# Performance work log

Hardware: AMD Instinct MI355X
Metric: run time of the kernel (lower is better)

## Reference

```python
import jax
import jax.numpy as jnp
import numpy as np

H = 16  # n_heads
EPS = 1e-6


def setup_inputs() -> dict:
    key = jax.random.key(0)
    ks = jax.random.split(key, 7)
    B, L, D = 2, 1024, 1024
    w_scale = 1.0 / np.sqrt(D)
    return {
        "query": jax.random.normal(ks[0], (B, L, D), jnp.float32),
        "key": jax.random.normal(ks[1], (B, L, D), jnp.float32),
        "value": jax.random.normal(ks[2], (B, L, D), jnp.float32),
        "Wq": jax.random.normal(ks[3], (D, D), jnp.float32) * w_scale,
        "Wk": jax.random.normal(ks[4], (D, D), jnp.float32) * w_scale,
        "Wv": jax.random.normal(ks[5], (D, D), jnp.float32) * w_scale,
        "Wo": jax.random.normal(ks[6], (D, D), jnp.float32) * w_scale,
    }


def _phi(x):
    # elu feature map: elu(x) + 1 (always positive)
    return jax.nn.elu(x) + 1.0


def reference(query, key, value, Wq, Wk, Wv, Wo):
    B, L, D = query.shape
    d = D // H
    scale = d ** -0.5

    def proj(x, W):
        # [B,L,D] -> [B,H,L,d]
        return (x @ W.T).reshape(B, L, H, d).transpose(0, 2, 1, 3)

    q = proj(query, Wq) * scale
    k = proj(key, Wk) * scale
    v = proj(value, Wv)

    qp = _phi(q)  # [B,H,L,d]
    kp = _phi(k)

    # causal linear attention as a recurrence over time (same math as the
    # torch cumsum of k outer v, but without materializing [B,H,L,d,d])
    qs = jnp.moveaxis(qp, 2, 0)  # [L,B,H,d]
    ks = jnp.moveaxis(kp, 2, 0)
    vs = jnp.moveaxis(v, 2, 0)

    S0 = jnp.zeros((B, H, d, d), query.dtype)  # running sum of k outer v
    z0 = jnp.zeros((B, H, d), query.dtype)     # running sum of k'

    def step(carry, inp):
        S, z = carry
        qt, kt, vt = inp
        S = S + kt[..., :, None] * vt[..., None, :]  # [B,H,d,d]
        z = z + kt
        num = jnp.einsum('bhd,bhde->bhe', qt, S)
        den = jnp.einsum('bhd,bhd->bh', qt, z)[..., None]
        return (S, z), num / (den + EPS)

    _, out = jax.lax.scan(step, (S0, z0), (qs, ks, vs))  # out: [L,B,H,d]
    out = jnp.moveaxis(out, 0, 1).reshape(B, L, D)  # [B,L,D]
    # dropout is identity in eval mode
    return out @ Wo.T
```

## Files before the change

kernel.cpp:

```cpp
#include <hip/hip_runtime.h>
#include <hip/hip_bf16.h>
#include <math.h>

#define H_HEADS 16
#define DMODEL  1024
#define DHEAD   64
#define LSEQ    1024
#define CHUNK   64
#define NCHUNK  16
#define EPS_F   1e-6f

typedef __attribute__((ext_vector_type(8))) short bf16x8;
typedef __attribute__((ext_vector_type(4))) float f32x4;

__device__ inline unsigned short f2bf(float f) {
    unsigned int u = __float_as_uint(f);
    u += 0x7FFF + ((u >> 16) & 1);
    return (unsigned short)(u >> 16);
}
__device__ inline float bf2f(unsigned short h) {
    return __uint_as_float(((unsigned int)h) << 16);
}

__device__ inline int swz16(int row, int byteInRow) {
    return row * 128 + (byteInRow ^ ((row & 7) << 4));
}

#define GLOAD16(g, l) __builtin_amdgcn_global_load_lds( \
    (const __attribute__((address_space(1))) void*)(g), \
    (__attribute__((address_space(3))) void*)(l), 16, 0, 0)

__global__ __launch_bounds__(256)
void convert_kernel(const float* __restrict__ q, const float* __restrict__ k,
                    const float* __restrict__ v,
                    const float* __restrict__ Wq, const float* __restrict__ Wk,
                    const float* __restrict__ Wv, const float* __restrict__ Wo,
                    unsigned short* __restrict__ Xb, unsigned short* __restrict__ Wb)
{
    const int y = blockIdx.y;
    const float* src;
    unsigned short* dst;
    int n;
    if (y < 3) {
        src = (y == 0) ? q : (y == 1) ? k : v;
        dst = Xb + (size_t)y * (2 * LSEQ * DMODEL);
        n = 2 * LSEQ * DMODEL;
    } else {
        int w = y - 3;
        src = (w == 0) ? Wq : (w == 1) ? Wk : (w == 2) ? Wv : Wo;
        dst = Wb + (size_t)w * (DMODEL * DMODEL);
        n = DMODEL * DMODEL;
    }
    int idx = (blockIdx.x * 256 + threadIdx.x) * 4;
    if (idx < n) {
        float4 f = *(const float4*)(src + idx);
        ushort4 h = make_ushort4(f2bf(f.x), f2bf(f.y), f2bf(f.z), f2bf(f.w));
        *(ushort4*)(dst + idx) = h;
    }
}

template<bool PROJ>
__global__ __launch_bounds__(256)
void mfma_gemm64_kernel(const unsigned short* __restrict__ Xb,
                        const unsigned short* __restrict__ Wb,
                        unsigned short* __restrict__ qp,
                        unsigned short* __restrict__ kp,
                        unsigned short* __restrict__ vp,
                        float* __restrict__ outf)
{
    const int z = PROJ ? blockIdx.z : 0;
    const unsigned short* X = PROJ ? (Xb + (size_t)z * (2 * LSEQ * DMODEL)) : Xb;
    const unsigned short* W = PROJ ? (Wb + (size_t)z * (DMODEL * DMODEL)) : Wb;

    __shared__ unsigned short As[2 * 64 * 32];
    __shared__ unsigned short Bs[2 * 128 * 32];

    const int tid  = threadIdx.x;
    const int m0   = blockIdx.y * 64;
    const int n0   = blockIdx.x * 128;
    const int lane = tid & 63;
    const int wid  = tid >> 6;
    const int wm   = (wid >> 1) * 32;
    const int wn   = (wid & 1) * 64;
    const int r16  = lane & 15;
    const int qh   = lane >> 4;

    const int rA  = wid * 16 + (lane >> 2);
    const int rB0 = wid * 32 + (lane >> 2);
    const int sw  = ((lane & 3) ^ ((lane >> 3) & 3)) * 16;
    const char* srcA  = (const char*)(X + (size_t)(m0 + rA)  * DMODEL) + sw;
    const char* srcB0 = (const char*)(W + (size_t)(n0 + rB0) * DMODEL) + sw;
    const char* srcB1 = (const char*)(W + (size_t)(n0 + rB0 + 16) * DMODEL) + sw;
    char* dstA  = (char*)As + wid * 1024;
    char* dstB0 = (char*)Bs + wid * 2048;
    char* dstB1 = (char*)Bs + wid * 2048 + 1024;

    const int sl = (qh ^ ((r16 >> 1) & 3)) * 8;

    f32x4 acc[2][4];
#pragma unroll
    for (int i = 0; i < 2; ++i)
#pragma unroll
        for (int j = 0; j < 4; ++j) acc[i][j] = (f32x4)0.0f;

    for (int kt = 0; kt < DMODEL; kt += 64) {
#pragma unroll
        for (int hh = 0; hh < 2; ++hh) {
            size_t go = (size_t)(kt + hh * 32) * 2;
            GLOAD16(srcA  + go, dstA  + hh * 4096);
            GLOAD16(srcB0 + go, dstB0 + hh * 8192);
            GLOAD16(srcB1 + go, dstB1 + hh * 8192);
        }
        __syncthreads();

        bf16x8 af[2][2], bg[2][4];
#pragma unroll
        for (int hh = 0; hh < 2; ++hh) {
#pragma unroll
            for (int fm = 0; fm < 2; ++fm)
                af[hh][fm] = *(const bf16x8*)&As[hh * 2048 + (wm + fm * 16 + r16) * 32 + sl];
#pragma unroll
            for (int fn = 0; fn < 4; ++fn)
                bg[hh][fn] = *(const bf16x8*)&Bs[hh * 4096 + (wn + fn * 16 + r16) * 32 + sl];
        }
#pragma unroll
        for (int hh = 0; hh < 2; ++hh)
#pragma unroll
            for (int fm = 0; fm < 2; ++fm)
#pragma unroll
                for (int fn = 0; fn < 4; ++fn)
                    acc[fm][fn] = __builtin_amdgcn_mfma_f32_16x16x32_bf16(
                        af[hh][fm], bg[hh][fn], acc[fm][fn], 0, 0, 0);
        __syncthreads();
    }

    if (PROJ) {
        unsigned short* O = (z == 0) ? qp : (z == 1) ? kp : vp;
        const float sc = (z < 2) ? 0.125f : 1.f;
#pragma unroll
        for (int fm = 0; fm < 2; ++fm) {
#pragma unroll
            for (int r = 0; r < 4; ++r) {
                int m = m0 + wm + fm * 16 + qh * 4 + r;
                int b = m >> 10, l = m & 1023;
#pragma unroll
                for (int fn = 0; fn < 4; ++fn) {
                    int n = n0 + wn + fn * 16 + r16;
                    int h = n >> 6, e = n & 63;
                    float y = acc[fm][fn][r] * sc;
                    if (z < 2) y = (y > 0.f) ? y + 1.f : __expf(y);
                    O[(((size_t)(b * H_HEADS + h)) * LSEQ + l) * DHEAD + e] = f2bf(y);
                }
            }
        }
    } else {
#pragma unroll
        for (int fm = 0; fm < 2; ++fm) {
#pragma unroll
            for (int r = 0; r < 4; ++r) {
                int m = m0 + wm + fm * 16 + qh * 4 + r;
#pragma unroll
                for (int fn = 0; fn < 4; ++fn) {
                    int n = n0 + wn + fn * 16 + r16;
                    outf[(size_t)m * DMODEL + n] = acc[fm][fn][r];
                }
            }
        }
    }
}

__global__ __launch_bounds__(256)
void chunk_kv_kernel(const unsigned short* __restrict__ kp,
                     const unsigned short* __restrict__ vp,
                     float* __restrict__ St, float* __restrict__ z)
{
    const int c = blockIdx.x, bh = blockIdx.y;
    const int tid = threadIdx.x;
    const int lane = tid & 63;
    const int w = tid >> 6;
    const int r16 = lane & 15, qh = lane >> 4;

    __shared__ unsigned short kT[64 * 64];
    __shared__ unsigned short vt[64 * 64];

    const size_t base = ((size_t)bh * LSEQ + (size_t)c * CHUNK) * DHEAD;

#pragma unroll
    for (int i = 0; i < 2; ++i) {
        int id  = tid + i * 256;
        int row = id >> 3;
        int cg  = (id & 7) * 8;
        bf16x8 kv = *(const bf16x8*)(kp + base + row * 64 + cg);
        bf16x8 vv = *(const bf16x8*)(vp + base + row * 64 + cg);
#pragma unroll
        for (int j = 0; j < 8; ++j) {
            *(unsigned short*)((char*)kT + swz16(cg + j, row * 2)) = (unsigned short)kv[j];
            *(unsigned short*)((char*)vt + swz16(cg + j, row * 2)) = (unsigned short)vv[j];
        }
    }
    __syncthreads();

    bf16x8 av[2], bK[2][4];
#pragma unroll
    for (int kk = 0; kk < 2; ++kk) {
        av[kk] = *(const bf16x8*)((char*)vt + swz16(w * 16 + r16, kk * 64 + qh * 16));
#pragma unroll
        for (int fn = 0; fn < 4; ++fn)
            bK[kk][fn] = *(const bf16x8*)((char*)kT + swz16(fn * 16 + r16, kk * 64 + qh * 16));
    }

    f32x4 acc[4];
#pragma unroll
    for (int fn = 0; fn < 4; ++fn) acc[fn] = (f32x4)0.0f;
#pragma unroll
    for (int kk = 0; kk < 2; ++kk)
#pragma unroll
        for (int fn = 0; fn < 4; ++fn)
            acc[fn] = __builtin_amdgcn_mfma_f32_16x16x32_bf16(av[kk], bK[kk][fn], acc[fn], 0, 0, 0);

    const size_t sbase = ((size_t)bh * NCHUNK + c) * (DHEAD * DHEAD);
#pragma unroll
    for (int r = 0; r < 4; ++r) {
        int e = w * 16 + qh * 4 + r;
#pragma unroll
        for (int fn = 0; fn < 4; ++fn)
            St[sbase + (size_t)e * 64 + fn * 16 + r16] = acc[fn][r];
    }

    if (w == 0) {
        bf16x8 ones;
#pragma unroll
        for (int j = 0; j < 8; ++j) ones[j] = (short)0x3F80;
        f32x4 accz[4];
#pragma unroll
        for (int fn = 0; fn < 4; ++fn) accz[fn] = (f32x4)0.0f;
#pragma unroll
        for (int kk = 0; kk < 2; ++kk)
#pragma unroll
            for (int fn = 0; fn < 4; ++fn)
                accz[fn] = __builtin_amdgcn_mfma_f32_16x16x32_bf16(ones, bK[kk][fn], accz[fn], 0, 0, 0);
        if (qh == 0) {
            const size_t zb = ((size_t)bh * NCHUNK + c) * 64;
#pragma unroll
            for (int fn = 0; fn < 4; ++fn)
                z[zb + fn * 16 + r16] = accz[fn][0];
        }
    }
}

__global__ __launch_bounds__(256)
void prefix_kernel(const float* __restrict__ St, unsigned short* __restrict__ stb,
                   float* __restrict__ z)
{
    const int bh   = blockIdx.x >> 4;
    const int eblk = blockIdx.x & 15;
    const int idx  = eblk * 256 + threadIdx.x;
    const int e = idx >> 6, i = idx & 63;

    const size_t ibase = (size_t)bh * NCHUNK * 4096 + idx;
    float v[NCHUNK];
#pragma unroll
    for (int c = 0; c < NCHUNK; ++c)
        v[c] = St[ibase + (size_t)c * 4096];

    const size_t obase = (size_t)bh * NCHUNK * 4096 + e * 64 + (i ^ ((e & 7) << 3));
    float run = 0.f;
#pragma unroll
    for (int c = 0; c < NCHUNK; ++c) {
        stb[obase + (size_t)c * 4096] = f2bf(run);
        run += v[c];
    }

    if (eblk == 0 && threadIdx.x < DHEAD) {
        const size_t zb = (size_t)bh * NCHUNK * DHEAD + threadIdx.x;
        float zv[NCHUNK];
#pragma unroll
        for (int c = 0; c < NCHUNK; ++c)
            zv[c] = z[zb + (size_t)c * DHEAD];
        float zr = 0.f;
#pragma unroll
        for (int c = 0; c < NCHUNK; ++c) {
            z[zb + (size_t)c * DHEAD] = zr;
            zr += zv[c];
        }
    }
}

__global__ __launch_bounds__(256)
void attn_mfma_kernel(const unsigned short* __restrict__ qp,
                      const unsigned short* __restrict__ kp,
                      const unsigned short* __restrict__ vp,
                      const unsigned short* __restrict__ stb,
                      const float* __restrict__ zpre,
                      unsigned short* __restrict__ att)
{
    const int c = blockIdx.x, bh = blockIdx.y;
    const int b = bh >> 4, h = bh & 15;
    const int tid = threadIdx.x;
    const int lane = tid & 63;
    const int w = tid >> 6;
    const int r16 = lane & 15, qh = lane >> 4;

    __shared__ unsigned short qs[64 * 64];
    __shared__ unsigned short ks[64 * 64];
    __shared__ unsigned short vt[64 * 64];
    __shared__ unsigned short stl[64 * 64];
    __shared__ unsigned short ps[64 * 64];
    __shared__ float denl[64];

    const size_t base = ((size_t)bh * LSEQ + (size_t)c * CHUNK) * DHEAD;
    const unsigned short* stg = stb + ((size_t)bh * NCHUNK + c) * 4096;
    const float* zp = zpre + ((size_t)bh * NCHUNK + c) * 64;

    {
        const char* src = (const char*)stg + w * 2048 + lane * 16;
        GLOAD16(src,        (char*)stl + w * 2048);
        GLOAD16(src + 1024, (char*)stl + w * 2048 + 1024);
    }
#pragma unroll
    for (int i = 0; i < 2; ++i) {
        int id  = tid + i * 256;
        int row = id >> 3;
        int cg  = (id & 7) * 8;
        bf16x8 qv = *(const bf16x8*)(qp + base + row * 64 + cg);
        bf16x8 kv = *(const bf16x8*)(kp + base + row * 64 + cg);
        *(bf16x8*)((char*)qs + swz16(row, cg * 2)) = qv;
        *(bf16x8*)((char*)ks + swz16(row, cg * 2)) = kv;
        bf16x8 vv = *(const bf16x8*)(vp + base + row * 64 + cg);
#pragma unroll
        for (int j = 0; j < 8; ++j)
            *(unsigned short*)((char*)vt + swz16(cg + j, row * 2)) = (unsigned short)vv[j];
    }
    {
        int t = tid >> 2, kq = tid & 3;
        const unsigned short* qrow = qp + base + t * 64 + kq * 16;
        bf16x8 a0 = *(const bf16x8*)(qrow);
        bf16x8 a1 = *(const bf16x8*)(qrow + 8);
        float s = 0.f;
#pragma unroll
        for (int j = 0; j < 8; ++j) {
            s = fmaf(bf2f((unsigned short)a0[j]), zp[kq * 16 + j], s);
            s = fmaf(bf2f((unsigned short)a1[j]), zp[kq * 16 + 8 + j], s);
        }
        s += __shfl_xor(s, 1);
        s += __shfl_xor(s, 2);
        if (kq == 0) denl[t] = s;
    }
    __syncthreads();

    bf16x8 aq[2];
#pragma unroll
    for (int kk = 0; kk < 2; ++kk)
        aq[kk] = *(const bf16x8*)((char*)qs + swz16(w * 16 + r16, kk * 64 + qh * 16));

    f32x4 accp[4];
#pragma unroll
    for (int fn = 0; fn < 4; ++fn) accp[fn] = (f32x4)0.0f;
#pragma unroll
    for (int kk = 0; kk < 2; ++kk)
#pragma unroll
        for (int fn = 0; fn < 4; ++fn) {
            bf16x8 bk = *(const bf16x8*)((char*)ks + swz16(fn * 16 + r16, kk * 64 + qh * 16));
            accp[fn] = __builtin_amdgcn_mfma_f32_16x16x32_bf16(aq[kk], bk, accp[fn], 0, 0, 0);
        }

    float rs[4];
#pragma unroll
    for (int r = 0; r < 4; ++r) {
        int t_loc = w * 16 + qh * 4 + r;
        float rsum = 0.f;
#pragma unroll
        for (int fn = 0; fn < 4; ++fn) {
            int s_loc = fn * 16 + r16;
            float p = (s_loc <= t_loc) ? accp[fn][r] : 0.f;
            rsum += p;
            *(unsigned short*)((char*)ps + swz16(t_loc, s_loc * 2)) = f2bf(p);
        }
        rsum += __shfl_xor(rsum, 1);
        rsum += __shfl_xor(rsum, 2);
        rsum += __shfl_xor(rsum, 4);
        rsum += __shfl_xor(rsum, 8);
        rs[r] = rsum;
    }

    f32x4 acc[4];
#pragma unroll
    for (int fn = 0; fn < 4; ++fn) acc[fn] = (f32x4)0.0f;
#pragma unroll
    for (int kk = 0; kk < 2; ++kk)
#pragma unroll
        for (int fn = 0; fn < 4; ++fn) {
            bf16x8 bs = *(const bf16x8*)((char*)stl + swz16(fn * 16 + r16, kk * 64 + qh * 16));
            acc[fn] = __builtin_amdgcn_mfma_f32_16x16x32_bf16(aq[kk], bs, acc[fn], 0, 0, 0);
        }
    bf16x8 ap[2];
#pragma unroll
    for (int kk = 0; kk < 2; ++kk)
        ap[kk] = *(const bf16x8*)((char*)ps + swz16(w * 16 + r16, kk * 64 + qh * 16));
#pragma unroll
    for (int kk = 0; kk < 2; ++kk)
#pragma unroll
        for (int fn = 0; fn < 4; ++fn) {
            bf16x8 bv = *(const bf16x8*)((char*)vt + swz16(fn * 16 + r16, kk * 64 + qh * 16));
            acc[fn] = __builtin_amdgcn_mfma_f32_16x16x32_bf16(ap[kk], bv, acc[fn], 0, 0, 0);
        }

#pragma unroll
    for (int r = 0; r < 4; ++r) {
        int t_loc = w * 16 + qh * 4 + r;
        int l = c * CHUNK + t_loc;
        float inv = 1.f / (denl[t_loc] + rs[r] + EPS_F);
#pragma unroll
        for (int fn = 0; fn < 4; ++fn) {
            int e = fn * 16 + r16;
            att[((size_t)b * LSEQ + l) * DMODEL + h * DHEAD + e] = f2bf(acc[fn][r] * inv);
        }
    }
}

extern "C" void kernel_launch(void* const* d_in, const int* in_sizes, int n_in,
                              void* d_out, int out_size, void* d_ws, size_t ws_size,
                              hipStream_t stream)
{
    const float* query = (const float*)d_in[0];
    const float* key_  = (const float*)d_in[1];
    const float* value = (const float*)d_in[2];
    const float* Wq = (const float*)d_in[3];
    const float* Wk = (const float*)d_in[4];
    const float* Wv = (const float*)d_in[5];
    const float* Wo = (const float*)d_in[6];
    float* out = (float*)d_out;

    const int M  = 2 * LSEQ;
    const int BH = 2 * H_HEADS;

    char* wsb = (char*)d_ws;
    unsigned short* Wb   = (unsigned short*)(wsb);
    unsigned short* qp   = (unsigned short*)(wsb + 8388608);
    unsigned short* kp   = (unsigned short*)(wsb + 12582912);
    unsigned short* vp   = (unsigned short*)(wsb + 16777216);
    unsigned short* attb = (unsigned short*)(wsb + 20971520);
    unsigned short* Xb   = (unsigned short*)(wsb + 25165824);
    float*          St   = (float*)(wsb + 25165824);
    float*          z    = (float*)(wsb + 33554432);
    unsigned short* stb  = (unsigned short*)(wsb + 33685504);

    dim3 blk(256);
    convert_kernel<<<dim3(2048, 7), blk, 0, stream>>>(
        query, key_, value, Wq, Wk, Wv, Wo, Xb, Wb);
    mfma_gemm64_kernel<true><<<dim3(DMODEL / 128, M / 64, 3), blk, 0, stream>>>(
        Xb, Wb, qp, kp, vp, nullptr);
    chunk_kv_kernel<<<dim3(NCHUNK, BH), blk, 0, stream>>>(kp, vp, St, z);
    prefix_kernel<<<dim3(BH * 16), blk, 0, stream>>>(St, stb, z);
    attn_mfma_kernel<<<dim3(NCHUNK, BH), blk, 0, stream>>>(qp, kp, vp, stb, z, attb);
    mfma_gemm64_kernel<false><<<dim3(DMODEL / 128, M / 64, 1), blk, 0, stream>>>(
        attb, Wb + 3 * (size_t)DMODEL * DMODEL, nullptr, nullptr, nullptr, out);
}
```

Measured before the change: 74.78 us.

## Double-buffer LDS tiles in MFMA GEMM to overlap global loads with compute

Splits the shared-memory A/B tiles into two buffers and issues direct global-to-LDS loads for the next K tile before running the MFMA work on the current one, with a single barrier per iteration. This is meant to hide global load latency behind matrix math in the projection and output GEMMs. It doubles LDS use per block, which may lower occupancy, and relies on hand-placed waitcnt and scheduling barriers being correct.

```diff
diff --git a/kernel.cpp b/kernel.cpp
--- a/kernel.cpp
+++ b/kernel.cpp
@@ -72,8 +72,8 @@
     const unsigned short* X = PROJ ? (Xb + (size_t)z * (2 * LSEQ * DMODEL)) : Xb;
     const unsigned short* W = PROJ ? (Wb + (size_t)z * (DMODEL * DMODEL)) : Wb;
 
-    __shared__ unsigned short As[2 * 64 * 32];
-    __shared__ unsigned short Bs[2 * 128 * 32];
+    __shared__ char AsB[2][8192];
+    __shared__ char BsB[2][16384];
 
     const int tid  = threadIdx.x;
     const int m0   = blockIdx.y * 64;
@@ -91,9 +91,6 @@
     const char* srcA  = (const char*)(X + (size_t)(m0 + rA)  * DMODEL) + sw;
     const char* srcB0 = (const char*)(W + (size_t)(n0 + rB0) * DMODEL) + sw;
     const char* srcB1 = (const char*)(W + (size_t)(n0 + rB0 + 16) * DMODEL) + sw;
-    char* dstA  = (char*)As + wid * 1024;
-    char* dstB0 = (char*)Bs + wid * 2048;
-    char* dstB1 = (char*)Bs + wid * 2048 + 1024;
 
     const int sl = (qh ^ ((r16 >> 1) & 3)) * 8;
 
@@ -103,25 +100,27 @@
 #pragma unroll
         for (int j = 0; j < 4; ++j) acc[i][j] = (f32x4)0.0f;
 
-    for (int kt = 0; kt < DMODEL; kt += 64) {
+    auto STAGE = [&](int buf, int kt) {
 #pragma unroll
         for (int hh = 0; hh < 2; ++hh) {
             size_t go = (size_t)(kt + hh * 32) * 2;
-            GLOAD16(srcA  + go, dstA  + hh * 4096);
-            GLOAD16(srcB0 + go, dstB0 + hh * 8192);
-            GLOAD16(srcB1 + go, dstB1 + hh * 8192);
-        }
-        __syncthreads();
-
+            GLOAD16(srcA  + go, AsB[buf] + wid * 1024 + hh * 4096);
+            GLOAD16(srcB0 + go, BsB[buf] + wid * 2048 + hh * 8192);
+            GLOAD16(srcB1 + go, BsB[buf] + wid * 2048 + 1024 + hh * 8192);
+        }
+    };
+    auto COMPUTE = [&](int buf) {
         bf16x8 af[2][2], bg[2][4];
 #pragma unroll
         for (int hh = 0; hh < 2; ++hh) {
 #pragma unroll
             for (int fm = 0; fm < 2; ++fm)
-                af[hh][fm] = *(const bf16x8*)&As[hh * 2048 + (wm + fm * 16 + r16) * 32 + sl];
+                af[hh][fm] = *(const bf16x8*)(AsB[buf] + hh * 4096 +
+                                 ((wm + fm * 16 + r16) * 32 + sl) * 2);
 #pragma unroll
             for (int fn = 0; fn < 4; ++fn)
-                bg[hh][fn] = *(const bf16x8*)&Bs[hh * 4096 + (wn + fn * 16 + r16) * 32 + sl];
+                bg[hh][fn] = *(const bf16x8*)(BsB[buf] + hh * 8192 +
+                                 ((wn + fn * 16 + r16) * 32 + sl) * 2);
         }
 #pragma unroll
         for (int hh = 0; hh < 2; ++hh)
@@ -131,8 +130,24 @@
                 for (int fn = 0; fn < 4; ++fn)
                     acc[fm][fn] = __builtin_amdgcn_mfma_f32_16x16x32_bf16(
                         af[hh][fm], bg[hh][fn], acc[fm][fn], 0, 0, 0);
-        __syncthreads();
-    }
+    };
+
+    STAGE(0, 0);
+    asm volatile("s_waitcnt vmcnt(0)" ::: "memory");
+    __builtin_amdgcn_s_barrier();
+
+    int cur = 0;
+#pragma unroll 1
+    for (int t = 0; t < (DMODEL / 64) - 1; ++t) {
+        STAGE(cur ^ 1, (t + 1) * 64);
+        __builtin_amdgcn_sched_barrier(0);
+        COMPUTE(cur);
+        asm volatile("s_waitcnt vmcnt(0) lgkmcnt(0)" ::: "memory");
+        __builtin_amdgcn_sched_barrier(0);
+        __builtin_amdgcn_s_barrier();
+        cur ^= 1;
+    }
+    COMPUTE(cur);
 
     if (PROJ) {
         unsigned short* O = (z == 0) ? qp : (z == 1) ? kp : vp;
```

Result: no change. 74.27 us (-0.7%).
